# Optimization experiments

Measured on AMD Instinct MI355X. Metric: run time of the kernel, lower is better.

## Reference

```python
import jax, jax.numpy as jnp
import numpy as np

N_NODES = 50000
N_EDGES = 600000
H = 128


def setup_inputs() -> dict:
    key = jax.random.key(0)
    ks = jax.random.split(key, 6)
    x = jax.random.normal(ks[0], (N_NODES, H), dtype=jnp.float32)
    edge_index = jax.random.randint(ks[1], (2, N_EDGES), 0, N_NODES, dtype=jnp.int64)
    edge_attr = jax.random.normal(ks[2], (N_EDGES, H), dtype=jnp.float32)
    # torch Linear-style params: weight (out, in), bias (out,)
    W1 = jax.random.normal(ks[3], (2 * H, 3 * H), dtype=jnp.float32) * (1.0 / np.sqrt(3 * H))
    b1 = jnp.zeros((2 * H,), dtype=jnp.float32)
    W2 = jax.random.normal(ks[4], (H, 2 * H), dtype=jnp.float32) * (1.0 / np.sqrt(2 * H))
    b2 = jnp.zeros((H,), dtype=jnp.float32)
    return {"x": x, "edge_index": edge_index, "edge_attr": edge_attr,
            "W1": W1, "b1": b1, "W2": W2, "b2": b2}


def reference(x, edge_index, edge_attr, W1, b1, W2, b2):
    row, col = edge_index[0], edge_index[1]
    # gather endpoint features and concat with edge features: [E, 3H]
    out = jnp.concatenate([x[row], x[col], edge_attr], axis=-1)
    h = jax.nn.relu(jnp.einsum('ef,gf->eg', out, W1) + b1)  # [E, 2H]
    return jnp.einsum('eg,hg->eh', h, W2) + b2              # [E, H]
```

## Files before the change

kernel.cpp:

```cpp
#include <hip/hip_runtime.h>
#include <hip/hip_fp16.h>

#define N_NODES 50000
#define N_EDGES 600000

typedef _Float16 f16x8 __attribute__((ext_vector_type(8)));
typedef _Float16 f16x4 __attribute__((ext_vector_type(4)));
typedef float f32x4 __attribute__((ext_vector_type(4)));

#define W1AB_OFF 0
#define W1C_OFF  65536
#define W2_OFF   98304
#define XAB_OFF  131072

__global__ __launch_bounds__(256) void convert_weights(
    const float* __restrict__ W1, const float* __restrict__ W2,
    _Float16* __restrict__ ws16) {
  int i = blockIdx.x * 256 + threadIdx.x;
  if (i < 65536) {
    int n = i >> 7, k = i & 127;
    float v = (n < 256) ? W1[n * 384 + k] : W1[(n - 256) * 384 + 128 + k];
    ws16[W1AB_OFF + i] = (_Float16)v;
  } else if (i < 98304) {
    int j = i - 65536;
    int n = j >> 7, k = j & 127;
    ws16[W1C_OFF + j] = (_Float16)W1[n * 384 + 256 + k];
  } else {
    int j = i - 98304;
    ws16[W2_OFF + j] = (_Float16)W2[j];
  }
}

__global__ __launch_bounds__(256, 2) void node_precompute(
    const float* __restrict__ x, _Float16* __restrict__ ws16) {
  const _Float16* __restrict__ w1ab = ws16 + W1AB_OFF;
  _Float16* __restrict__ xab = ws16 + XAB_OFF;

  __shared__ __align__(16) _Float16 xt[64][136];
  int tid = threadIdx.x;
  int v0 = blockIdx.x * 64;

#pragma unroll
  for (int it = 0; it < 8; ++it) {
    int f = tid + it * 256;
    int r = f >> 5;
    int c = (f & 31) * 4;
    int vr = v0 + r;
    if (vr > N_NODES - 1) vr = N_NODES - 1;
    float4 val = *(const float4*)&x[(size_t)vr * 128 + c];
    f16x4 h;
    h[0] = (_Float16)val.x; h[1] = (_Float16)val.y;
    h[2] = (_Float16)val.z; h[3] = (_Float16)val.w;
    *(f16x4*)&xt[r][c] = h;
  }
  __syncthreads();

  int lane = tid & 63;
  int w = tid >> 6;
  int m16 = lane & 15;
  int quad = lane >> 4;

  for (int nn = 0; nn < 2; ++nn) {
    f32x4 acc[4][4] = {};
#pragma unroll
    for (int kk = 0; kk < 4; ++kk) {
      f16x8 a[4];
#pragma unroll
      for (int m = 0; m < 4; ++m)
        a[m] = *(const f16x8*)&xt[m * 16 + m16][kk * 32 + quad * 8];
#pragma unroll
      for (int j = 0; j < 4; ++j) {
        int n = w * 128 + nn * 64 + j * 16 + m16;
        f16x8 b = *(const f16x8*)&w1ab[n * 128 + kk * 32 + quad * 8];
#pragma unroll
        for (int m = 0; m < 4; ++m)
          acc[m][j] = __builtin_amdgcn_mfma_f32_16x16x32_f16(a[m], b, acc[m][j], 0, 0, 0);
      }
    }
#pragma unroll
    for (int m = 0; m < 4; ++m)
#pragma unroll
      for (int j = 0; j < 4; ++j)
#pragma unroll
        for (int r = 0; r < 4; ++r) {
          int v = v0 + m * 16 + quad * 4 + r;
          if (v < N_NODES) {
            int n = w * 128 + nn * 64 + j * 16 + m16;
            xab[(size_t)v * 512 + n] = (_Float16)acc[m][j][r];
          }
        }
  }
}

__global__ __launch_bounds__(256, 3) void edge_mlp(
    const int* __restrict__ ei, const float* __restrict__ ea,
    const float* __restrict__ b1, const float* __restrict__ b2,
    const _Float16* __restrict__ ws16, float* __restrict__ out) {
  const _Float16* __restrict__ w1c = ws16 + W1C_OFF;
  const _Float16* __restrict__ w2h = ws16 + W2_OFF;
  const _Float16* __restrict__ xab = ws16 + XAB_OFF;

  __shared__ __align__(16) _Float16 eat[64][136];
  __shared__ __align__(16) _Float16 sh[64][264];
  __shared__ int eidx[128];

  int tid = threadIdx.x;
  int e0 = blockIdx.x * 64;

  if (tid < 128) {
    int which = tid >> 6;
    int el = tid & 63;
    int v = ei[(size_t)which * N_EDGES + e0 + el];
    if (v < 0) v = 0;
    if (v > N_NODES - 1) v = N_NODES - 1;
    eidx[tid] = v;
  }
  __syncthreads();

  int lane = tid & 63;
  int w = tid >> 6;

#pragma unroll
  for (int it = 0; it < 8; ++it) {
    int f = tid + it * 256;
    int r = f >> 5;
    int c = (f & 31) * 4;
    float4 val = *(const float4*)&ea[(size_t)(e0 + r) * 128 + c];
    f16x4 h;
    h[0] = (_Float16)val.x; h[1] = (_Float16)val.y;
    h[2] = (_Float16)val.z; h[3] = (_Float16)val.w;
    *(f16x4*)&eat[r][c] = h;
  }

  {
    float4 bb = *(const float4*)&b1[lane * 4];
#pragma unroll 4
    for (int i = 0; i < 16; ++i) {
      int el = w * 16 + i;
      int vr = eidx[el];
      int vc = eidx[64 + el];
      f16x4 va = *(const f16x4*)&xab[(size_t)vr * 512 + lane * 4];
      f16x4 vb = *(const f16x4*)&xab[(size_t)vc * 512 + 256 + lane * 4];
      f16x4 s;
      s[0] = (_Float16)((float)va[0] + (float)vb[0] + bb.x);
      s[1] = (_Float16)((float)va[1] + (float)vb[1] + bb.y);
      s[2] = (_Float16)((float)va[2] + (float)vb[2] + bb.z);
      s[3] = (_Float16)((float)va[3] + (float)vb[3] + bb.w);
      *(f16x4*)&sh[el][lane * 4] = s;
    }
  }
  __syncthreads();

  int m16 = lane & 15;
  int quad = lane >> 4;

  f32x4 acc[4][4] = {};
#pragma unroll
  for (int kk = 0; kk < 4; ++kk) {
    f16x8 a[4];
#pragma unroll
    for (int m = 0; m < 4; ++m)
      a[m] = *(const f16x8*)&eat[m * 16 + m16][kk * 32 + quad * 8];
#pragma unroll
    for (int j = 0; j < 4; ++j) {
      int n = w * 64 + j * 16 + m16;
      f16x8 b = *(const f16x8*)&w1c[n * 128 + kk * 32 + quad * 8];
#pragma unroll
      for (int m = 0; m < 4; ++m)
        acc[m][j] = __builtin_amdgcn_mfma_f32_16x16x32_f16(a[m], b, acc[m][j], 0, 0, 0);
    }
  }

#pragma unroll
  for (int m = 0; m < 4; ++m)
#pragma unroll
    for (int j = 0; j < 4; ++j) {
      int c = w * 64 + j * 16 + m16;
#pragma unroll
      for (int r = 0; r < 4; ++r) {
        int row = m * 16 + quad * 4 + r;
        float v = acc[m][j][r] + (float)sh[row][c];
        v = v > 0.f ? v : 0.f;
        sh[row][c] = (_Float16)v;
      }
    }
  __syncthreads();

  f32x4 acc2[4][2] = {};
#pragma unroll
  for (int kk = 0; kk < 8; ++kk) {
    f16x8 a[4];
#pragma unroll
    for (int m = 0; m < 4; ++m)
      a[m] = *(const f16x8*)&sh[m * 16 + m16][kk * 32 + quad * 8];
#pragma unroll
    for (int j = 0; j < 2; ++j) {
      int n = w * 32 + j * 16 + m16;
      f16x8 b = *(const f16x8*)&w2h[n * 256 + kk * 32 + quad * 8];
#pragma unroll
      for (int m = 0; m < 4; ++m)
        acc2[m][j] = __builtin_amdgcn_mfma_f32_16x16x32_f16(a[m], b, acc2[m][j], 0, 0, 0);
    }
  }

#pragma unroll
  for (int m = 0; m < 4; ++m)
#pragma unroll
    for (int j = 0; j < 2; ++j) {
      int n = w * 32 + j * 16 + m16;
      float bias = b2[n];
#pragma unroll
      for (int r = 0; r < 4; ++r) {
        int e = e0 + m * 16 + quad * 4 + r;
        out[(size_t)e * 128 + n] = acc2[m][j][r] + bias;
      }
    }
}

extern "C" void kernel_launch(void* const* d_in, const int* in_sizes, int n_in,
                              void* d_out, int out_size, void* d_ws, size_t ws_size,
                              hipStream_t stream) {
  const float* x  = (const float*)d_in[0];
  const int*   ei = (const int*)d_in[1];
  const float* ea = (const float*)d_in[2];
  const float* W1 = (const float*)d_in[3];
  const float* b1 = (const float*)d_in[4];
  const float* W2 = (const float*)d_in[5];
  const float* b2 = (const float*)d_in[6];
  float* out = (float*)d_out;
  _Float16* ws16 = (_Float16*)d_ws;

  convert_weights<<<512, 256, 0, stream>>>(W1, W2, ws16);
  node_precompute<<<(N_NODES + 63) / 64, 256, 0, stream>>>(x, ws16);
  edge_mlp<<<N_EDGES / 64, 256, 0, stream>>>(ei, ea, b1, b2, ws16, out);
}
```

Baseline: 683.0 us.

## Load edge features directly into MFMA fragments and transpose node precompute stores

The edge kernel no longer stages edge_attr through shared memory. Each lane loads the fp32 values its MFMA A-fragment needs straight from global memory and converts them to fp16 in registers. This frees LDS for higher occupancy (launch bounds raised to 4 blocks) and removes one barrier phase. The node precompute swaps operand roles so each lane writes contiguous f16x4 vectors instead of scattered scalar halves, and output stores become nontemporal. The direct global reads are less coalesced per instruction and may re-fetch cache lines.

```diff
diff --git a/kernel.cpp b/kernel.cpp
--- a/kernel.cpp
+++ b/kernel.cpp
@@ -60,39 +60,33 @@
   int m16 = lane & 15;
   int quad = lane >> 4;
 
-  for (int nn = 0; nn < 2; ++nn) {
-    f32x4 acc[4][4] = {};
-#pragma unroll
-    for (int kk = 0; kk < 4; ++kk) {
-      f16x8 a[4];
-#pragma unroll
-      for (int m = 0; m < 4; ++m)
-        a[m] = *(const f16x8*)&xt[m * 16 + m16][kk * 32 + quad * 8];
-#pragma unroll
-      for (int j = 0; j < 4; ++j) {
-        int n = w * 128 + nn * 64 + j * 16 + m16;
-        f16x8 b = *(const f16x8*)&w1ab[n * 128 + kk * 32 + quad * 8];
-#pragma unroll
-        for (int m = 0; m < 4; ++m)
-          acc[m][j] = __builtin_amdgcn_mfma_f32_16x16x32_f16(a[m], b, acc[m][j], 0, 0, 0);
-      }
-    }
-#pragma unroll
-    for (int m = 0; m < 4; ++m)
-#pragma unroll
-      for (int j = 0; j < 4; ++j)
-#pragma unroll
-        for (int r = 0; r < 4; ++r) {
-          int v = v0 + m * 16 + quad * 4 + r;
-          if (v < N_NODES) {
-            int n = w * 128 + nn * 64 + j * 16 + m16;
-            xab[(size_t)v * 512 + n] = (_Float16)acc[m][j][r];
-          }
-        }
-  }
-}
-
-__global__ __launch_bounds__(256, 3) void edge_mlp(
+  int v = v0 + m16;
+  for (int nn = 0; nn < 8; ++nn) {
+    int nb = w * 128 + nn * 16;
+    f16x8 afr[4];
+#pragma unroll
+    for (int kk = 0; kk < 4; ++kk)
+      afr[kk] = *(const f16x8*)&w1ab[(size_t)(nb + m16) * 128 + kk * 32 + quad * 8];
+#pragma unroll
+    for (int vb = 0; vb < 4; ++vb) {
+      f32x4 acc = {};
+#pragma unroll
+      for (int kk = 0; kk < 4; ++kk) {
+        f16x8 b = *(const f16x8*)&xt[vb * 16 + m16][kk * 32 + quad * 8];
+        acc = __builtin_amdgcn_mfma_f32_16x16x32_f16(afr[kk], b, acc, 0, 0, 0);
+      }
+      int vv = v + vb * 16;
+      if (vv < N_NODES) {
+        f16x4 hv;
+        hv[0] = (_Float16)acc[0]; hv[1] = (_Float16)acc[1];
+        hv[2] = (_Float16)acc[2]; hv[3] = (_Float16)acc[3];
+        *(f16x4*)&xab[(size_t)vv * 512 + nb + quad * 4] = hv;
+      }
+    }
+  }
+}
+
+__global__ __launch_bounds__(256, 4) void edge_mlp(
     const int* __restrict__ ei, const float* __restrict__ ea,
     const float* __restrict__ b1, const float* __restrict__ b2,
     const _Float16* __restrict__ ws16, float* __restrict__ out) {
@@ -100,7 +94,6 @@
   const _Float16* __restrict__ w2h = ws16 + W2_OFF;
   const _Float16* __restrict__ xab = ws16 + XAB_OFF;
 
-  __shared__ __align__(16) _Float16 eat[64][136];
   __shared__ __align__(16) _Float16 sh[64][264];
   __shared__ int eidx[128];
 
@@ -119,18 +112,8 @@
 
   int lane = tid & 63;
   int w = tid >> 6;
-
-#pragma unroll
-  for (int it = 0; it < 8; ++it) {
-    int f = tid + it * 256;
-    int r = f >> 5;
-    int c = (f & 31) * 4;
-    float4 val = *(const float4*)&ea[(size_t)(e0 + r) * 128 + c];
-    f16x4 h;
-    h[0] = (_Float16)val.x; h[1] = (_Float16)val.y;
-    h[2] = (_Float16)val.z; h[3] = (_Float16)val.w;
-    *(f16x4*)&eat[r][c] = h;
-  }
+  int m16 = lane & 15;
+  int quad = lane >> 4;
 
   {
     float4 bb = *(const float4*)&b1[lane * 4];
@@ -149,27 +132,33 @@
       *(f16x4*)&sh[el][lane * 4] = s;
     }
   }
-  __syncthreads();
-
-  int m16 = lane & 15;
-  int quad = lane >> 4;
 
   f32x4 acc[4][4] = {};
 #pragma unroll
   for (int kk = 0; kk < 4; ++kk) {
     f16x8 a[4];
 #pragma unroll
-    for (int m = 0; m < 4; ++m)
-      a[m] = *(const f16x8*)&eat[m * 16 + m16][kk * 32 + quad * 8];
+    for (int m = 0; m < 4; ++m) {
+      const float* p = &ea[(size_t)(e0 + m * 16 + m16) * 128 + kk * 32 + quad * 8];
+      float4 u0 = *(const float4*)p;
+      float4 u1 = *(const float4*)(p + 4);
+      f16x8 av;
+      av[0] = (_Float16)u0.x; av[1] = (_Float16)u0.y;
+      av[2] = (_Float16)u0.z; av[3] = (_Float16)u0.w;
+      av[4] = (_Float16)u1.x; av[5] = (_Float16)u1.y;
+      av[6] = (_Float16)u1.z; av[7] = (_Float16)u1.w;
+      a[m] = av;
+    }
 #pragma unroll
     for (int j = 0; j < 4; ++j) {
       int n = w * 64 + j * 16 + m16;
-      f16x8 b = *(const f16x8*)&w1c[n * 128 + kk * 32 + quad * 8];
+      f16x8 b = *(const f16x8*)&w1c[(size_t)n * 128 + kk * 32 + quad * 8];
 #pragma unroll
       for (int m = 0; m < 4; ++m)
         acc[m][j] = __builtin_amdgcn_mfma_f32_16x16x32_f16(a[m], b, acc[m][j], 0, 0, 0);
     }
   }
+  __syncthreads();
 
 #pragma unroll
   for (int m = 0; m < 4; ++m)
@@ -196,7 +185,7 @@
 #pragma unroll
     for (int j = 0; j < 2; ++j) {
       int n = w * 32 + j * 16 + m16;
-      f16x8 b = *(const f16x8*)&w2h[n * 256 + kk * 32 + quad * 8];
+      f16x8 b = *(const f16x8*)&w2h[(size_t)n * 256 + kk * 32 + quad * 8];
 #pragma unroll
       for (int m = 0; m < 4; ++m)
         acc2[m][j] = __builtin_amdgcn_mfma_f32_16x16x32_f16(a[m], b, acc2[m][j], 0, 0, 0);
@@ -212,7 +201,7 @@
 #pragma unroll
       for (int r = 0; r < 4; ++r) {
         int e = e0 + m * 16 + quad * 4 + r;
-        out[(size_t)e * 128 + n] = acc2[m][j][r] + bias;
+        __builtin_nontemporal_store(acc2[m][j][r] + bias, &out[(size_t)e * 128 + n]);
       }
     }
 }
```

Result: slower. 816.8 us (+19.6%).
